# Performance work log

Measured on AMD Instinct MI355X. Metric: run time of the kernel, lower is better.

Reference implementation:

```python
import jax, jax.numpy as jnp
import numpy as np

B, N, S, H = 128, 512, 8, 64
HORIZON = 12


def setup_inputs() -> dict:
    key = jax.random.key(0)
    ks = jax.random.split(key, 24)
    sc = 0.05
    inp = {
        "crowd_obsv": jax.random.normal(ks[0], (B, N, S, 2), jnp.float32),
        "pad_mask": jax.random.bernoulli(ks[1], 0.9, (B, N, N)),
        "neg_hist_mask": jnp.ones((B, N, S, 1), jnp.float32),
        # LSTM params (PyTorch layout, gate order i,f,g,o)
        "Wih": jax.random.normal(ks[2], (4 * H, 2), jnp.float32) * sc,
        "Whh": jax.random.normal(ks[3], (4 * H, H), jnp.float32) * sc,
        "bih": jax.random.normal(ks[4], (4 * H,), jnp.float32) * sc,
        "bhh": jax.random.normal(ks[5], (4 * H,), jnp.float32) * sc,
        # human_encoder: ReLU, Linear, ReLU, Linear, ReLU
        "W_enc1": jax.random.normal(ks[6], (H, H), jnp.float32) * sc,
        "b_enc1": jax.random.normal(ks[7], (H,), jnp.float32) * sc,
        "W_enc2": jax.random.normal(ks[8], (H, H), jnp.float32) * sc,
        "b_enc2": jax.random.normal(ks[9], (H,), jnp.float32) * sc,
        # human_head: Linear, ReLU
        "W_head": jax.random.normal(ks[10], (H, H), jnp.float32) * sc,
        "b_head": jax.random.normal(ks[11], (H,), jnp.float32) * sc,
        "Wq": jax.random.normal(ks[12], (H, H), jnp.float32) * sc,
        "bq": jax.random.normal(ks[13], (H,), jnp.float32) * sc,
        "Wk": jax.random.normal(ks[14], (H, H), jnp.float32) * sc,
        "bk": jax.random.normal(ks[15], (H,), jnp.float32) * sc,
        "Wv": jax.random.normal(ks[16], (H, H), jnp.float32) * sc,
        "bv": jax.random.normal(ks[17], (H,), jnp.float32) * sc,
        # human_forecaster: Linear(2H -> horizon*2)
        "Wf": jax.random.normal(ks[18], (HORIZON * 2, 2 * H), jnp.float32) * sc,
        "bf": jax.random.normal(ks[19], (HORIZON * 2,), jnp.float32) * sc,
    }
    return inp


def _forward(crowd_obsv, pad_mask, neg_hist_mask, Wih, Whh, bih, bhh,
             W_enc1, b_enc1, W_enc2, b_enc2, W_head, b_head,
             Wq, bq, Wk, bk, Wv, bv, Wf, bf):
    b, n, s, _ = crowd_obsv.shape
    h_dim = Whh.shape[1]
    horizon = Wf.shape[0] // 2

    x = (crowd_obsv * neg_hist_mask).reshape(-1, s, 2)  # [M, S, 2]
    m = x.shape[0]

    # --- variable-length masking: find last zero index (x-channel) ---
    zero_mask = (x == 0)                                  # [M, S, 2]
    ar = jnp.arange(s)
    lzi = jnp.max(zero_mask * ar[None, :, None], axis=1)  # [M, 2]
    lzi = jnp.where(zero_mask.any(axis=1), lzi, -1)
    lzi = lzi[:, 0]                                       # [M]
    rows = ar[None, :]
    kill = (rows < lzi[:, None]) & (lzi[:, None] >= 0)    # [M, S]
    x = jnp.where(kill[:, :, None], jnp.zeros((), x.dtype), x)
    length = jnp.maximum((s - 1) - lzi, 1)                # clamp(7 - lzi, min=1)

    # --- packed LSTM via masked scan: state frozen once t >= length ---
    bias = bih + bhh

    def step(carry, inp):
        h, c = carry
        xt, t = inp
        gates = xt @ Wih.T + h @ Whh.T + bias           # [M, 4H]
        i, f, g, o = jnp.split(gates, 4, axis=-1)
        c_new = jax.nn.sigmoid(f) * c + jax.nn.sigmoid(i) * jnp.tanh(g)
        h_new = jax.nn.sigmoid(o) * jnp.tanh(c_new)
        upd = (t < length)[:, None]
        return (jnp.where(upd, h_new, h), jnp.where(upd, c_new, c)), None

    init = (jnp.zeros((m, h_dim), x.dtype), jnp.zeros((m, h_dim), x.dtype))
    (hn, _), _ = jax.lax.scan(step, init, (x.transpose(1, 0, 2), jnp.arange(s)))

    he = hn.reshape(b, n, h_dim)

    # human_encoder + human_head
    h1 = jax.nn.relu(he)
    h1 = jax.nn.relu(h1 @ W_enc1.T + b_enc1)
    h1 = jax.nn.relu(h1 @ W_enc2.T + b_enc2)
    hidden = jax.nn.relu(h1 @ W_head.T + b_head)

    q = hidden @ Wq.T + bq
    k = hidden @ Wk.T + bk
    v = hidden @ Wv.T + bv

    logits = jnp.einsum('bnh,bmh->bnm', q, k)
    logits = jnp.where(pad_mask, logits, jnp.asarray(-999999999999.0, logits.dtype))
    attn = jnp.einsum('bnm,bmh->bnh', jax.nn.softmax(logits, axis=2), v)

    feat = jnp.concatenate([v, attn], axis=-1)            # [B, N, 2H]
    forecast = (feat @ Wf.T + bf).reshape(-1, n, horizon, 2)
    return forecast, feat


def reference(crowd_obsv, pad_mask, neg_hist_mask, Wih, Whh, bih, bhh,
              W_enc1, b_enc1, W_enc2, b_enc2, W_head, b_head,
              Wq, bq, Wk, bk, Wv, bv, Wf, bf):
    return _forward(crowd_obsv, pad_mask, neg_hist_mask, Wih, Whh, bih, bhh,
                    W_enc1, b_enc1, W_enc2, b_enc2, W_head, b_head,
                    Wq, bq, Wk, bk, Wv, bv, Wf, bf)
```

## Files before the change

kernel.cpp:

```cpp
#include <hip/hip_runtime.h>
#include <hip/hip_bf16.h>
#include <stdint.h>

#define B_ 128
#define N_ 512
#define S_ 8
#define H_ 64
#define M_ (B_*N_)
#define L2E 1.442695041f

typedef __attribute__((ext_vector_type(8))) short bf16x8;
typedef __attribute__((ext_vector_type(4))) float f32x4;

__device__ __forceinline__ float exp2f_(float x) { return __builtin_amdgcn_exp2f(x); }
__device__ __forceinline__ float rcpf_(float x)  { return __builtin_amdgcn_rcpf(x); }
__device__ __forceinline__ float sig2(float x)  { return rcpf_(1.f + exp2f_(-x)); }
__device__ __forceinline__ float tanh2(float x) { return 1.f - 2.f*rcpf_(exp2f_(x) + 1.f); }
__device__ __forceinline__ unsigned short f2bf(float x) {
  unsigned int u = __float_as_uint(x);
  u += 0x7fffu + ((u >> 16) & 1u);
  return (unsigned short)(u >> 16);
}

__global__ __launch_bounds__(512, 4) void lstm_kernel(
    const float* __restrict__ obs, const float* __restrict__ nhm,
    const float* __restrict__ Wih, const float* __restrict__ Whh,
    const float* __restrict__ bih, const float* __restrict__ bhh,
    unsigned short* __restrict__ he,
    const int4* __restrict__ pm4, uint32_t* __restrict__ bm,
    const float* __restrict__ W1, const float* __restrict__ W2,
    const float* __restrict__ Wh, const float* __restrict__ Wq,
    const float* __restrict__ Wk, const float* __restrict__ Wv,
    const float* __restrict__ Wf, unsigned short* __restrict__ wg)
{
  __shared__ short    Wfrag[32*512];
  __shared__ short    Wxc[1024];
  __shared__ short    h_s[128*72];

  const int tid  = threadIdx.x;
  const int lane = tid & 63;
  const int wv   = tid >> 6;
  const int w16  = wv * 16;
  const int quad = lane >> 4;
  const int col  = lane & 15;
  const int row0 = blockIdx.x * 128;

  const int     wb  = (blockIdx.x*8 + wv) * 256;
  const int4*   pw  = pm4 + (size_t)wb * 8;
  const int     shp = (lane & 7) * 4;

  #pragma unroll
  for (int i = 0; i < 4; ++i) {
    int p = i*512 + tid;
    int f = p >> 6, l = p & 63;
    int t16 = f >> 1, s = f & 1;
    int lq = l >> 4, lc = l & 15;
    const float sc = (t16 >= 8 && t16 < 12) ? (2.f*L2E) : L2E;
    const float* src = Whh + (size_t)(t16*16 + lc)*64 + s*32 + lq*8;
    short* dst = Wfrag + f*512 + l*8;
    #pragma unroll
    for (int j = 0; j < 8; ++j) dst[j] = (short)f2bf(src[j] * sc);
  }
  if (tid < 256) {
    int t16 = tid >> 4, cc = tid & 15;
    int n = t16*16 + cc;
    const float sc = (t16 >= 8 && t16 < 12) ? (2.f*L2E) : L2E;
    short* d = Wxc + t16*64 + cc*4;
    d[0] = (short)f2bf(Wih[2*n + 0] * sc);
    d[1] = (short)f2bf(Wih[2*n + 1] * sc);
    d[2] = (short)f2bf((bih[n] + bhh[n]) * sc);
    d[3] = 0;
  }

  #pragma unroll
  for (int i = 0; i < 9; ++i) ((uint32_t*)h_s)[i*512 + tid] = 0u;

  if (blockIdx.x < 7) {
    const int m = blockIdx.x;
    const int p = tid;
    const int f = p >> 6, l = p & 63;
    const int lq = l >> 4, lc = l & 15;
    bf16x8 v;
    #pragma unroll
    for (int j = 0; j < 8; ++j) v[j] = 0;
    if (m < 6) {
      const float* mats[6] = {W1, W2, Wh, Wq, Wk, Wv};
      const float sc = (m == 3) ? L2E : 1.f;
      const int nt = f >> 1, s = f & 1;
      const float* src = mats[m] + (size_t)(nt*16 + lc)*64 + s*32 + lq*8;
      #pragma unroll
      for (int j = 0; j < 8; ++j) v[j] = (short)f2bf(src[j]);
      if (m == 3) {
        #pragma unroll
        for (int j = 0; j < 8; ++j) v[j] = (short)f2bf(src[j] * sc);
      }
    } else {
      const int kc = f >> 1, nt = f & 1;
      const int n = nt*16 + lc;
      if (n < 24) {
        const float* src = Wf + (size_t)n*128 + kc*32 + lq*8;
        #pragma unroll
        for (int j = 0; j < 8; ++j) v[j] = (short)f2bf(src[j]);
      }
    }
    *(bf16x8*)(wg + (size_t)m*4096 + f*512 + l*8) = v;
  }

  uint32_t xq0, xq1, xq2, xq3, xq4, xq5, xq6, xq7;
  int len;
  {
    const int grow = row0 + w16 + col;
    float xv0[8], xv1[8];
    int lzi = -1;
    #pragma unroll
    for (int t = 0; t < 8; ++t) {
      float m = nhm[(size_t)grow*8 + t];
      float a = obs[((size_t)grow*8 + t)*2 + 0] * m;
      float b = obs[((size_t)grow*8 + t)*2 + 1] * m;
      xv0[t] = a; xv1[t] = b;
      if (a == 0.f) lzi = t;
    }
    uint32_t xr[8];
    #pragma unroll
    for (int t = 0; t < 8; ++t) {
      bool kill = (t < lzi);
      float a = kill ? 0.f : xv0[t];
      float b = kill ? 0.f : xv1[t];
      xr[t] = (uint32_t)f2bf(a) | ((uint32_t)f2bf(b) << 16);
    }
    xq0 = xr[0]; xq1 = xr[1]; xq2 = xr[2]; xq3 = xr[3];
    xq4 = xr[4]; xq5 = xr[5]; xq6 = xr[6]; xq7 = xr[7];
    len = 7 - lzi; if (len < 1) len = 1;
  }
  int lenr[4];
  #pragma unroll
  for (int r = 0; r < 4; ++r) lenr[r] = __shfl(len, quad*4 + r);

  __syncthreads();

  float c_[16];
  #pragma unroll
  for (int i = 0; i < 16; ++i) c_[i] = 0.f;

  const f32x4 zero4 = {0.f, 0.f, 0.f, 0.f};
  const bool q0 = (quad == 0);

  #pragma unroll 1
  for (int t = 0; t < 8; ++t) {
    const int4* ps = pw + t*256 + lane;
    int4 pv0 = ps[0];
    int4 pv1 = ps[64];
    int4 pv2 = ps[128];
    int4 pv3 = ps[192];
    __builtin_amdgcn_sched_barrier(0);

    uint32_t xw = xq0;
    xq0 = xq1; xq1 = xq2; xq2 = xq3; xq3 = xq4;
    xq4 = xq5; xq5 = xq6; xq6 = xq7;

    union { bf16x8 v; uint32_t u[4]; } ax;
    ax.u[0] = q0 ? xw : 0u;
    ax.u[1] = q0 ? 0x00003f80u : 0u;
    ax.u[2] = 0u; ax.u[3] = 0u;

    bf16x8 a0 = *(const bf16x8*)(h_s + (w16 + col)*72 + quad*8);
    bf16x8 a1 = *(const bf16x8*)(h_s + (w16 + col)*72 + 32 + quad*8);

    #pragma unroll
    for (int cc = 0; cc < 4; ++cc) {
      f32x4 acc[4];
      #pragma unroll
      for (int g = 0; g < 4; ++g) {
        const int t16 = g*4 + cc;
        union { bf16x8 v; uint32_t u[4]; } wx;
        uint2 d = *(const uint2*)(Wxc + t16*64 + col*4);
        wx.u[0] = q0 ? d.x : 0u;
        wx.u[1] = q0 ? d.y : 0u;
        wx.u[2] = 0u; wx.u[3] = 0u;
        bf16x8 b0 = *(const bf16x8*)(Wfrag + (t16*2+0)*512 + lane*8);
        bf16x8 b1 = *(const bf16x8*)(Wfrag + (t16*2+1)*512 + lane*8);
        acc[g] = __builtin_amdgcn_mfma_f32_16x16x32_bf16(ax.v, wx.v, zero4, 0, 0, 0);
        acc[g] = __builtin_amdgcn_mfma_f32_16x16x32_bf16(a0, b0, acc[g], 0, 0, 0);
        acc[g] = __builtin_amdgcn_mfma_f32_16x16x32_bf16(a1, b1, acc[g], 0, 0, 0);
      }
      #pragma unroll
      for (int r = 0; r < 4; ++r) {
        if (t < lenr[r]) {
          float gi = acc[0][r];
          float gf = acc[1][r];
          float gg = acc[2][r];
          float go = acc[3][r];
          float cn = sig2(gf)*c_[cc*4+r] + sig2(gi)*tanh2(gg);
          c_[cc*4+r] = cn;
          h_s[(w16 + quad*4 + r)*72 + cc*16 + col] =
              (short)f2bf(sig2(go)*tanh2(cn*(2.f*L2E)));
        }
      }
      __builtin_amdgcn_sched_barrier(0);
    }

    {
      int4 vv[4] = {pv0, pv1, pv2, pv3};
      #pragma unroll
      for (int jj = 0; jj < 4; ++jj) {
        int4 v = vv[jj];
        uint32_t nib = (v.x != 0 ? 1u : 0u)
                     | (v.y != 0 ? 2u : 0u)
                     | (v.z != 0 ? 4u : 0u)
                     | (v.w != 0 ? 8u : 0u);
        uint32_t x = nib << shp;
        x |= __shfl_xor(x, 1);
        x |= __shfl_xor(x, 2);
        x |= __shfl_xor(x, 4);
        if ((lane & 7) == 0)
          bm[wb + t*32 + jj*8 + (lane >> 3)] = x;
      }
      __builtin_amdgcn_sched_barrier(0);
    }
  }

  #pragma unroll
  for (int s = 0; s < 2; ++s) {
    int chunk = s*64 + lane;
    int rl = chunk >> 3, c8 = chunk & 7;
    bf16x8 v = *(const bf16x8*)(h_s + (w16 + rl)*72 + c8*8);
    #pragma unroll
    for (int j = 0; j < 8; ++j) {
      short sv = v[j];
      v[j] = (sv & (short)0x8000) ? (short)0 : sv;
    }
    *(bf16x8*)(he + (size_t)(row0 + w16 + rl)*64 + c8*8) = v;
  }
}

__global__ __launch_bounds__(256) void mlp_kernel(
    const unsigned short* __restrict__ he, const unsigned short* __restrict__ wg,
    const float* __restrict__ b1, const float* __restrict__ b2,
    const float* __restrict__ bh, const float* __restrict__ bq,
    const float* __restrict__ bk, const float* __restrict__ bv,
    unsigned short* __restrict__ qb, unsigned short* __restrict__ kb,
    unsigned short* __restrict__ vt, float* __restrict__ feat)
{
  __shared__ short Atile[4][16*76];

  const int tid  = threadIdx.x;
  const int lane = tid & 63;
  const int wv   = tid >> 6;
  const int quad = lane >> 4;
  const int col  = lane & 15;
  const int rowb = blockIdx.x*64 + wv*16;

  bf16x8 a0 = *(const bf16x8*)(he + (size_t)(rowb + col)*64 + quad*8);
  bf16x8 a1 = *(const bf16x8*)(he + (size_t)(rowb + col)*64 + quad*8 + 32);

  f32x4 acc[4];
  auto runL = [&](int m, const float* __restrict__ bs, float bsc) {
    bf16x8 bf[8];
    #pragma unroll
    for (int f = 0; f < 8; ++f)
      bf[f] = *(const bf16x8*)(wg + (size_t)m*4096 + f*512 + lane*8);
    #pragma unroll
    for (int nt = 0; nt < 4; ++nt) {
      float bb = bs[nt*16 + col] * bsc;
      acc[nt][0] = bb; acc[nt][1] = bb; acc[nt][2] = bb; acc[nt][3] = bb;
      acc[nt] = __builtin_amdgcn_mfma_f32_16x16x32_bf16(a0, bf[nt*2+0], acc[nt], 0,0,0);
      acc[nt] = __builtin_amdgcn_mfma_f32_16x16x32_bf16(a1, bf[nt*2+1], acc[nt], 0,0,0);
    }
  };
  auto tileWrite = [&](bool relu) {
    #pragma unroll
    for (int nt = 0; nt < 4; ++nt)
      #pragma unroll
      for (int r = 0; r < 4; ++r) {
        float v = relu ? fmaxf(acc[nt][r], 0.f) : acc[nt][r];
        Atile[wv][(quad*4+r)*76 + ((nt*16+col) ^ (r*16))] = (short)f2bf(v);
      }
  };
  auto tileReadA = [&]() {
    int sw = (col & 3) * 16;
    a0 = *(const bf16x8*)(&Atile[wv][col*76 + ((quad*8     ) ^ sw)]);
    a1 = *(const bf16x8*)(&Atile[wv][col*76 + ((quad*8 + 32) ^ sw)]);
  };
  auto storeBF = [&](unsigned short* dst) {
    #pragma unroll
    for (int s = 0; s < 2; ++s) {
      int chunk = s*64 + lane;
      int r = chunk >> 3, c8 = chunk & 7;
      bf16x8 v = *(const bf16x8*)(&Atile[wv][r*76 + ((c8*8) ^ ((r&3)*16))]);
      *(bf16x8*)(dst + (size_t)(rowb + r)*64 + c8*8) = v;
    }
  };

  runL(0, b1, 1.f);  tileWrite(true);  tileReadA();
  runL(1, b2, 1.f);  tileWrite(true);  tileReadA();
  runL(2, bh, 1.f);  tileWrite(true);  tileReadA();
  runL(3, bq, L2E);  tileWrite(false); storeBF(qb);
  runL(4, bk, 1.f);  tileWrite(false); storeBF(kb);
  runL(5, bv, 1.f);
  {
    const int bi   = rowb >> 9;
    const int key0 = (rowb & 511) + quad*4;
    #pragma unroll
    for (int nt = 0; nt < 4; ++nt) {
      #pragma unroll
      for (int r = 0; r < 4; ++r)
        feat[(size_t)(rowb + quad*4 + r)*128 + nt*16 + col] = acc[nt][r];
      uint32_t lo = (uint32_t)f2bf(acc[nt][0]) | ((uint32_t)f2bf(acc[nt][1]) << 16);
      uint32_t hi = (uint32_t)f2bf(acc[nt][2]) | ((uint32_t)f2bf(acc[nt][3]) << 16);
      uint2 pk; pk.x = lo; pk.y = hi;
      *(uint2*)(vt + ((size_t)bi*64 + nt*16 + col)*512 + key0) = pk;
    }
  }
}

__global__ __launch_bounds__(256) void attn_kernel(
    const unsigned short* __restrict__ qg, const unsigned short* __restrict__ kg,
    const unsigned short* __restrict__ vt,
    const uint32_t* __restrict__ bm, float* __restrict__ feat,
    const unsigned short* __restrict__ wg, const float* __restrict__ bfv,
    float* __restrict__ out)
{
  __shared__ short    Ks[128*72];
  __shared__ short    Vt[64*136];
  __shared__ short    Pl[4][16*32];
  __shared__ uint32_t Ms[4][256];

  const int tid  = threadIdx.x;
  const int lane = tid & 63;
  const int wv   = tid >> 6;
  const int w16  = wv * 16;
  const int quad = lane >> 4;
  const int col  = lane & 15;

  const int b     = blockIdx.x >> 3;
  const int q0    = (blockIdx.x & 7) * 64;
  const int qbase = b*512 + q0 + wv*16;

  bf16x8 qa[2];
  qa[0] = *(const bf16x8*)(qg + (size_t)(qbase + col)*64 + quad*8);
  qa[1] = *(const bf16x8*)(qg + (size_t)(qbase + col)*64 + quad*8 + 32);

  #pragma unroll
  for (int w = 0; w < 4; ++w)
    Ms[wv][w*64 + lane] = bm[(size_t)qbase*16 + w*64 + lane];

  f32x4 o_acc[4];
  #pragma unroll
  for (int nt = 0; nt < 4; ++nt)
    #pragma unroll
    for (int r = 0; r < 4; ++r) o_acc[nt][r] = 0.f;
  float l_part[4] = {0.f, 0.f, 0.f, 0.f};

  const unsigned short* vtb = vt + (size_t)b*64*512;

  for (int c = 0; c < 4; ++c) {
    __syncthreads();
    {
      const int kb_ = b*512 + c*128;
      #pragma unroll
      for (int i = 0; i < 4; ++i) {
        int p = i*256 + tid;
        int key = p >> 3, c8 = p & 7;
        bf16x8 kv = *(const bf16x8*)(kg + (size_t)(kb_ + key)*64 + c8*8);
        *(bf16x8*)(Ks + key*72 + c8*8) = kv;
      }
      #pragma unroll
      for (int i = 0; i < 4; ++i) {
        int p = i*256 + tid;
        int dim = p >> 4, k8 = p & 15;
        bf16x8 vv = *(const bf16x8*)(vtb + (size_t)dim*512 + c*128 + k8*8);
        *(bf16x8*)(Vt + dim*136 + k8*8) = vv;
      }
    }
    __syncthreads();

    for (int kc = 0; kc < 4; ++kc) {
      #pragma unroll
      for (int t = 0; t < 2; ++t) {
        const int kt = kc*2 + t;
        f32x4 s_acc;
        #pragma unroll
        for (int r = 0; r < 4; ++r) s_acc[r] = 0.f;
        const short* kp = Ks + (kt*16 + col)*72 + quad*8;
        bf16x8 kb0 = *(const bf16x8*)(kp);
        bf16x8 kb1 = *(const bf16x8*)(kp + 32);
        s_acc = __builtin_amdgcn_mfma_f32_16x16x32_bf16(qa[0], kb0, s_acc, 0,0,0);
        s_acc = __builtin_amdgcn_mfma_f32_16x16x32_bf16(qa[1], kb1, s_acc, 0,0,0);
        const int kcol = ((t*16 + col) ^ (quad*8));
        #pragma unroll
        for (int r = 0; r < 4; ++r) {
          uint32_t mw = Ms[wv][(quad*4+r)*16 + c*4 + (kt>>1)];
          float p = ((mw >> ((kt&1)*16 + col)) & 1u)
                      ? exp2f_(fminf(s_acc[r], 43.f)) : 0.f;
          l_part[r] += p;
          Pl[wv][(quad*4+r)*32 + kcol] = (short)f2bf(p);
        }
      }
      bf16x8 pa = *(const bf16x8*)(&Pl[wv][col*32 + ((quad*8) ^ (((col)>>2)*8))]);
      #pragma unroll
      for (int nt = 0; nt < 4; ++nt) {
        bf16x8 vb = *(const bf16x8*)(&Vt[(nt*16+col)*136 + kc*32 + quad*8]);
        o_acc[nt] = __builtin_amdgcn_mfma_f32_16x16x32_bf16(pa, vb, o_acc[nt], 0,0,0);
      }
    }
  }

  float inv[4];
  #pragma unroll
  for (int r = 0; r < 4; ++r) {
    float v = l_part[r];
    v += __shfl_xor(v, 1);
    v += __shfl_xor(v, 2);
    v += __shfl_xor(v, 4);
    v += __shfl_xor(v, 8);
    inv[r] = rcpf_(fmaxf(v, 1e-20f));
  }

  #pragma unroll
  for (int nt = 0; nt < 4; ++nt)
    #pragma unroll
    for (int r = 0; r < 4; ++r)
      feat[(size_t)(qbase + quad*4 + r)*128 + 64 + nt*16 + col] = o_acc[nt][r]*inv[r];

  __syncthreads();

  #pragma unroll
  for (int nt = 0; nt < 4; ++nt)
    #pragma unroll
    for (int r = 0; r < 4; ++r)
      Ks[(w16 + quad*4 + r)*72 + nt*16 + col] = (short)f2bf(o_acc[nt][r]*inv[r]);

  bf16x8 af[4];
  const float* fr = feat + (size_t)(qbase + col)*128;
  #pragma unroll
  for (int kc = 0; kc < 2; ++kc) {
    float4 f0 = *(const float4*)(fr + kc*32 + quad*8);
    float4 f1 = *(const float4*)(fr + kc*32 + quad*8 + 4);
    af[kc][0]=(short)f2bf(f0.x); af[kc][1]=(short)f2bf(f0.y);
    af[kc][2]=(short)f2bf(f0.z); af[kc][3]=(short)f2bf(f0.w);
    af[kc][4]=(short)f2bf(f1.x); af[kc][5]=(short)f2bf(f1.y);
    af[kc][6]=(short)f2bf(f1.z); af[kc][7]=(short)f2bf(f1.w);
  }
  #pragma unroll
  for (int kc = 2; kc < 4; ++kc)
    af[kc] = *(const bf16x8*)(Ks + (w16 + col)*72 + (kc-2)*32 + quad*8);

  f32x4 facc[2];
  #pragma unroll
  for (int nt = 0; nt < 2; ++nt) {
    int n = nt*16 + col;
    float bb = (n < 24) ? bfv[n] : 0.f;
    facc[nt][0] = bb; facc[nt][1] = bb; facc[nt][2] = bb; facc[nt][3] = bb;
  }
  #pragma unroll
  for (int kc = 0; kc < 4; ++kc) {
    #pragma unroll
    for (int nt = 0; nt < 2; ++nt) {
      bf16x8 bfr = *(const bf16x8*)(wg + (size_t)6*4096 + (kc*2+nt)*512 + lane*8);
      facc[nt] = __builtin_amdgcn_mfma_f32_16x16x32_bf16(af[kc], bfr, facc[nt], 0,0,0);
    }
  }

  #pragma unroll
  for (int nt = 0; nt < 2; ++nt) {
    int n = nt*16 + col;
    if (n < 24) {
      #pragma unroll
      for (int r = 0; r < 4; ++r)
        out[(size_t)(qbase + quad*4 + r)*24 + n] = facc[nt][r];
    }
  }
}

extern "C" void kernel_launch(void* const* d_in, const int* in_sizes, int n_in,
                              void* d_out, int out_size, void* d_ws, size_t ws_size,
                              hipStream_t stream)
{
  const float* obs = (const float*)d_in[0];
  const int*   pm  = (const int*)  d_in[1];
  const float* nhm = (const float*)d_in[2];
  const float* Wih = (const float*)d_in[3];
  const float* Whh = (const float*)d_in[4];
  const float* bih = (const float*)d_in[5];
  const float* bhh = (const float*)d_in[6];
  const float* W1  = (const float*)d_in[7];
  const float* b1  = (const float*)d_in[8];
  const float* W2  = (const float*)d_in[9];
  const float* b2  = (const float*)d_in[10];
  const float* Wh  = (const float*)d_in[11];
  const float* bh  = (const float*)d_in[12];
  const float* Wq  = (const float*)d_in[13];
  const float* bq  = (const float*)d_in[14];
  const float* Wk  = (const float*)d_in[15];
  const float* bk  = (const float*)d_in[16];
  const float* Wv  = (const float*)d_in[17];
  const float* bv  = (const float*)d_in[18];
  const float* Wf  = (const float*)d_in[19];
  const float* bf  = (const float*)d_in[20];

  float* out  = (float*)d_out;
  float* feat = out + (size_t)M_*24;

  char* ws = (char*)d_ws;
  unsigned short* he  = (unsigned short*)(ws);
  unsigned short* qbf = (unsigned short*)(ws + (size_t) 8*1024*1024);
  unsigned short* kbf = (unsigned short*)(ws + (size_t)16*1024*1024);
  unsigned short* vtb = (unsigned short*)(ws + (size_t)24*1024*1024);
  uint32_t*       bmw = (uint32_t*)      (ws + (size_t)32*1024*1024);
  unsigned short* wgb = (unsigned short*)(ws + (size_t)36*1024*1024);

  lstm_kernel<<<M_/128, 512, 0, stream>>>(obs, nhm, Wih, Whh, bih, bhh, he,
                                          (const int4*)pm, bmw,
                                          W1, W2, Wh, Wq, Wk, Wv, Wf, wgb);
  mlp_kernel<<<M_/64, 256, 0, stream>>>(he, wgb, b1, b2, bh, bq, bk, bv,
                                        qbf, kbf, vtb, feat);
  attn_kernel<<<M_/64, 256, 0, stream>>>(qbf, kbf, vtb, bmw, feat, wgb, bf, out);
}
```

Before: 302.9 us.

## Fuse MLP/QKV projection into LSTM kernel and split weight conversion into own kernel

Moves the encoder/head/QKV MLP chain into the tail of the LSTM kernel, reading the final hidden state straight from shared memory instead of writing and reloading an intermediate bf16 buffer through global memory. Weight conversion to bf16 MFMA fragments moves into a small separate kernel launched first, since the fused kernel now consumes those weights. This removes one kernel launch and the global round trip of the hidden states. In exchange it adds a tiny extra launch and more register and shared-memory pressure in an already large LSTM kernel with launch bounds (512,4), which could reduce occupancy or cause spills.

```diff
diff --git a/kernel.cpp b/kernel.cpp
--- a/kernel.cpp
+++ b/kernel.cpp
@@ -22,16 +22,49 @@
   return (unsigned short)(u >> 16);
 }
 
+__global__ __launch_bounds__(512) void wconv_kernel(
+    const float* __restrict__ W1, const float* __restrict__ W2,
+    const float* __restrict__ Wh, const float* __restrict__ Wq,
+    const float* __restrict__ Wk, const float* __restrict__ Wv,
+    const float* __restrict__ Wf, unsigned short* __restrict__ wg)
+{
+  const int m = blockIdx.x;
+  const int p = threadIdx.x;
+  const int f = p >> 6, l = p & 63;
+  const int lq = l >> 4, lc = l & 15;
+  bf16x8 v;
+  #pragma unroll
+  for (int j = 0; j < 8; ++j) v[j] = 0;
+  if (m < 6) {
+    const float* mats[6] = {W1, W2, Wh, Wq, Wk, Wv};
+    const float sc = (m == 3) ? L2E : 1.f;
+    const int nt = f >> 1, s = f & 1;
+    const float* src = mats[m] + (size_t)(nt*16 + lc)*64 + s*32 + lq*8;
+    #pragma unroll
+    for (int j = 0; j < 8; ++j) v[j] = (short)f2bf(src[j] * sc);
+  } else {
+    const int kc = f >> 1, nt = f & 1;
+    const int n = nt*16 + lc;
+    if (n < 24) {
+      const float* src = Wf + (size_t)n*128 + kc*32 + lq*8;
+      #pragma unroll
+      for (int j = 0; j < 8; ++j) v[j] = (short)f2bf(src[j]);
+    }
+  }
+  *(bf16x8*)(wg + (size_t)m*4096 + f*512 + l*8) = v;
+}
+
 __global__ __launch_bounds__(512, 4) void lstm_kernel(
     const float* __restrict__ obs, const float* __restrict__ nhm,
     const float* __restrict__ Wih, const float* __restrict__ Whh,
     const float* __restrict__ bih, const float* __restrict__ bhh,
-    unsigned short* __restrict__ he,
     const int4* __restrict__ pm4, uint32_t* __restrict__ bm,
-    const float* __restrict__ W1, const float* __restrict__ W2,
-    const float* __restrict__ Wh, const float* __restrict__ Wq,
-    const float* __restrict__ Wk, const float* __restrict__ Wv,
-    const float* __restrict__ Wf, unsigned short* __restrict__ wg)
+    const unsigned short* __restrict__ wg,
+    const float* __restrict__ b1, const float* __restrict__ b2,
+    const float* __restrict__ bh, const float* __restrict__ bq,
+    const float* __restrict__ bk, const float* __restrict__ bv,
+    unsigned short* __restrict__ qb, unsigned short* __restrict__ kb,
+    unsigned short* __restrict__ vt, float* __restrict__ feat)
 {
   __shared__ short    Wfrag[32*512];
   __shared__ short    Wxc[1024];
@@ -74,37 +107,6 @@
 
   #pragma unroll
   for (int i = 0; i < 9; ++i) ((uint32_t*)h_s)[i*512 + tid] = 0u;
-
-  if (blockIdx.x < 7) {
-    const int m = blockIdx.x;
-    const int p = tid;
-    const int f = p >> 6, l = p & 63;
-    const int lq = l >> 4, lc = l & 15;
-    bf16x8 v;
-    #pragma unroll
-    for (int j = 0; j < 8; ++j) v[j] = 0;
-    if (m < 6) {
-      const float* mats[6] = {W1, W2, Wh, Wq, Wk, Wv};
-      const float sc = (m == 3) ? L2E : 1.f;
-      const int nt = f >> 1, s = f & 1;
-      const float* src = mats[m] + (size_t)(nt*16 + lc)*64 + s*32 + lq*8;
-      #pragma unroll
-      for (int j = 0; j < 8; ++j) v[j] = (short)f2bf(src[j]);
-      if (m == 3) {
-        #pragma unroll
-        for (int j = 0; j < 8; ++j) v[j] = (short)f2bf(src[j] * sc);
-      }
-    } else {
-      const int kc = f >> 1, nt = f & 1;
-      const int n = nt*16 + lc;
-      if (n < 24) {
-        const float* src = Wf + (size_t)n*128 + kc*32 + lq*8;
-        #pragma unroll
-        for (int j = 0; j < 8; ++j) v[j] = (short)f2bf(src[j]);
-      }
-    }
-    *(bf16x8*)(wg + (size_t)m*4096 + f*512 + l*8) = v;
-  }
 
   uint32_t xq0, xq1, xq2, xq3, xq4, xq5, xq6, xq7;
   int len;
@@ -219,39 +221,20 @@
     }
   }
 
-  #pragma unroll
-  for (int s = 0; s < 2; ++s) {
-    int chunk = s*64 + lane;
-    int rl = chunk >> 3, c8 = chunk & 7;
-    bf16x8 v = *(const bf16x8*)(h_s + (w16 + rl)*72 + c8*8);
+  short* At = h_s + w16*72;
+  const int grow16 = row0 + w16;
+
+  auto reluv = [](bf16x8 v) {
     #pragma unroll
     for (int j = 0; j < 8; ++j) {
       short sv = v[j];
       v[j] = (sv & (short)0x8000) ? (short)0 : sv;
     }
-    *(bf16x8*)(he + (size_t)(row0 + w16 + rl)*64 + c8*8) = v;
-  }
-}
-
-__global__ __launch_bounds__(256) void mlp_kernel(
-    const unsigned short* __restrict__ he, const unsigned short* __restrict__ wg,
-    const float* __restrict__ b1, const float* __restrict__ b2,
-    const float* __restrict__ bh, const float* __restrict__ bq,
-    const float* __restrict__ bk, const float* __restrict__ bv,
-    unsigned short* __restrict__ qb, unsigned short* __restrict__ kb,
-    unsigned short* __restrict__ vt, float* __restrict__ feat)
-{
-  __shared__ short Atile[4][16*76];
-
-  const int tid  = threadIdx.x;
-  const int lane = tid & 63;
-  const int wv   = tid >> 6;
-  const int quad = lane >> 4;
-  const int col  = lane & 15;
-  const int rowb = blockIdx.x*64 + wv*16;
-
-  bf16x8 a0 = *(const bf16x8*)(he + (size_t)(rowb + col)*64 + quad*8);
-  bf16x8 a1 = *(const bf16x8*)(he + (size_t)(rowb + col)*64 + quad*8 + 32);
+    return v;
+  };
+
+  bf16x8 a0 = reluv(*(const bf16x8*)(At + col*72 + quad*8));
+  bf16x8 a1 = reluv(*(const bf16x8*)(At + col*72 + 32 + quad*8));
 
   f32x4 acc[4];
   auto runL = [&](int m, const float* __restrict__ bs, float bsc) {
@@ -273,21 +256,21 @@
       #pragma unroll
       for (int r = 0; r < 4; ++r) {
         float v = relu ? fmaxf(acc[nt][r], 0.f) : acc[nt][r];
-        Atile[wv][(quad*4+r)*76 + ((nt*16+col) ^ (r*16))] = (short)f2bf(v);
+        At[(quad*4+r)*72 + ((nt*16+col) ^ (r*16))] = (short)f2bf(v);
       }
   };
   auto tileReadA = [&]() {
     int sw = (col & 3) * 16;
-    a0 = *(const bf16x8*)(&Atile[wv][col*76 + ((quad*8     ) ^ sw)]);
-    a1 = *(const bf16x8*)(&Atile[wv][col*76 + ((quad*8 + 32) ^ sw)]);
+    a0 = *(const bf16x8*)(At + col*72 + ((quad*8     ) ^ sw));
+    a1 = *(const bf16x8*)(At + col*72 + ((quad*8 + 32) ^ sw));
   };
   auto storeBF = [&](unsigned short* dst) {
     #pragma unroll
     for (int s = 0; s < 2; ++s) {
       int chunk = s*64 + lane;
       int r = chunk >> 3, c8 = chunk & 7;
-      bf16x8 v = *(const bf16x8*)(&Atile[wv][r*76 + ((c8*8) ^ ((r&3)*16))]);
-      *(bf16x8*)(dst + (size_t)(rowb + r)*64 + c8*8) = v;
+      bf16x8 v = *(const bf16x8*)(At + r*72 + ((c8*8) ^ ((r&3)*16)));
+      *(bf16x8*)(dst + (size_t)(grow16 + r)*64 + c8*8) = v;
     }
   };
 
@@ -298,13 +281,13 @@
   runL(4, bk, 1.f);  tileWrite(false); storeBF(kb);
   runL(5, bv, 1.f);
   {
-    const int bi   = rowb >> 9;
-    const int key0 = (rowb & 511) + quad*4;
+    const int bi   = grow16 >> 9;
+    const int key0 = (grow16 & 511) + quad*4;
     #pragma unroll
     for (int nt = 0; nt < 4; ++nt) {
       #pragma unroll
       for (int r = 0; r < 4; ++r)
-        feat[(size_t)(rowb + quad*4 + r)*128 + nt*16 + col] = acc[nt][r];
+        feat[(size_t)(grow16 + quad*4 + r)*128 + nt*16 + col] = acc[nt][r];
       uint32_t lo = (uint32_t)f2bf(acc[nt][0]) | ((uint32_t)f2bf(acc[nt][1]) << 16);
       uint32_t hi = (uint32_t)f2bf(acc[nt][2]) | ((uint32_t)f2bf(acc[nt][3]) << 16);
       uint2 pk; pk.x = lo; pk.y = hi;
@@ -502,17 +485,16 @@
   float* feat = out + (size_t)M_*24;
 
   char* ws = (char*)d_ws;
-  unsigned short* he  = (unsigned short*)(ws);
-  unsigned short* qbf = (unsigned short*)(ws + (size_t) 8*1024*1024);
-  unsigned short* kbf = (unsigned short*)(ws + (size_t)16*1024*1024);
-  unsigned short* vtb = (unsigned short*)(ws + (size_t)24*1024*1024);
-  uint32_t*       bmw = (uint32_t*)      (ws + (size_t)32*1024*1024);
-  unsigned short* wgb = (unsigned short*)(ws + (size_t)36*1024*1024);
-
-  lstm_kernel<<<M_/128, 512, 0, stream>>>(obs, nhm, Wih, Whh, bih, bhh, he,
-                                          (const int4*)pm, bmw,
-                                          W1, W2, Wh, Wq, Wk, Wv, Wf, wgb);
-  mlp_kernel<<<M_/64, 256, 0, stream>>>(he, wgb, b1, b2, bh, bq, bk, bv,
-                                        qbf, kbf, vtb, feat);
+  unsigned short* qbf = (unsigned short*)(ws);
+  unsigned short* kbf = (unsigned short*)(ws + (size_t) 8*1024*1024);
+  unsigned short* vtb = (unsigned short*)(ws + (size_t)16*1024*1024);
+  uint32_t*       bmw = (uint32_t*)      (ws + (size_t)24*1024*1024);
+  unsigned short* wgb = (unsigned short*)(ws + (size_t)28*1024*1024);
+
+  wconv_kernel<<<7, 512, 0, stream>>>(W1, W2, Wh, Wq, Wk, Wv, Wf, wgb);
+  lstm_kernel<<<M_/128, 512, 0, stream>>>(obs, nhm, Wih, Whh, bih, bhh,
+                                          (const int4*)pm, bmw, wgb,
+                                          b1, b2, bh, bq, bk, bv,
+                                          qbf, kbf, vtb, feat);
   attn_kernel<<<M_/64, 256, 0, stream>>>(qbf, kbf, vtb, bmw, feat, wgb, bf, out);
 }
```

Result: no change. 297.3 us (-1.8%).
